# Kernel optimization log

Hardware: AMD Instinct MI355X
Metric: run time of the kernel (lower is better)

## Reference

```python
import jax, jax.numpy as jnp
import numpy as np

EPS = 1e-5

def _bn(x, g, b, m, v):
    # inference-mode batchnorm over channel axis 1
    s = (1, -1) + (1,) * (x.ndim - 2)
    return (x - m.reshape(s)) * (g.reshape(s) / jnp.sqrt(v.reshape(s) + EPS)) + b.reshape(s)

def _lrelu(x):
    return jnp.where(x >= 0, x, 0.2 * x)

def _graph_feature(x, k):
    # x: (B, C, N) -> (B, 2C, N, k): DGCNN cat([neighbor - center, center])
    xt = jnp.transpose(x, (0, 2, 1))                      # (B, N, C)
    sq = jnp.sum(xt * xt, axis=-1)                        # (B, N)
    neg_dist = 2.0 * jnp.einsum('bnc,bmc->bnm', xt, xt) - sq[:, :, None] - sq[:, None, :]
    idx = jax.lax.top_k(neg_dist, k)[1]                   # (B, N, k) nearest (incl. self)
    nb = jax.vmap(lambda f, i: f[i])(xt, idx)             # (B, N, k, C) neighbor gather
    ctr = jnp.broadcast_to(xt[:, :, None, :], nb.shape)
    feat = jnp.concatenate([nb - ctr, ctr], axis=-1)      # (B, N, k, 2C)
    return jnp.transpose(feat, (0, 3, 1, 2))

def _edge_conv(x, k, w, g, b, m, v):
    # 1x1 conv over edge features + BN + LeakyReLU(0.2) + max over k neighbors
    f = _graph_feature(x, k)
    h = jnp.einsum('oi,bink->bonk', w, f)
    return jnp.max(_lrelu(_bn(h, g, b, m, v)), axis=-1)   # (B, out, N)

def setup_inputs():
    key = jax.random.key(0)
    ks = jax.random.split(key, 40)
    rn = lambda i, s: jax.random.normal(ks[i], s, dtype=jnp.float32)
    ru = lambda i, s: jax.random.uniform(ks[i], s, dtype=jnp.float32)
    B, N, K = 8, 1024, 20
    inp = {'x': rn(0, (B, N, 3))}
    dims = [(64, 6), (64, 128), (128, 128), (256, 256)]
    for li, (o, ci) in enumerate(dims, 1):
        base = li * 5
        inp[f'c{li}w'] = rn(base, (o, ci)) * 0.2
        inp[f'c{li}g'] = ru(base + 1, (o,)) + 0.5
        inp[f'c{li}b'] = rn(base + 2, (o,)) * 0.1
        inp[f'c{li}m'] = rn(base + 3, (o,)) * 0.1
        inp[f'c{li}v'] = ru(base + 4, (o,)) + 0.5
    inp['f1w'] = rn(25, (128, 384)) * 0.05
    inp['f1b'] = rn(26, (128,)) * 0.1
    inp['n1g'] = ru(27, (128,)) + 0.5
    inp['n1b'] = rn(28, (128,)) * 0.1
    inp['n1m'] = rn(29, (128,)) * 0.1
    inp['n1v'] = ru(30, (128,)) + 0.5
    inp['f2w'] = rn(31, (16, 128)) * 0.1
    inp['f2b'] = rn(32, (16,)) * 0.1
    inp['n2g'] = ru(33, (16,)) + 0.5
    inp['n2b'] = rn(34, (16,)) * 0.1
    inp['n2m'] = rn(35, (16,)) * 0.1
    inp['n2v'] = ru(36, (16,)) + 0.5
    inp['f3w'] = rn(37, (1, 16)) * 0.2
    inp['f3b'] = rn(38, (1,)) * 0.1
    inp['k'] = K
    return inp

def reference(x, c1w, c1g, c1b, c1m, c1v, c2w, c2g, c2b, c2m, c2v,
              c3w, c3g, c3b, c3m, c3v, c4w, c4g, c4b, c4m, c4v,
              f1w, f1b, n1g, n1b, n1m, n1v, f2w, f2b, n2g, n2b, n2m, n2v,
              f3w, f3b, k):
    xt = jnp.transpose(x, (0, 2, 1))                       # (B, 3, N)
    h1 = _edge_conv(xt, k, c1w, c1g, c1b, c1m, c1v)        # (B, 64, N)
    h2 = _edge_conv(h1, k, c2w, c2g, c2b, c2m, c2v)        # (B, 64, N)
    h3 = _edge_conv(h2, k, c3w, c3g, c3b, c3m, c3v)        # (B, 128, N)
    h4 = _edge_conv(h3, k, c4w, c4g, c4b, c4m, c4v)        # (B, 256, N)
    p3 = jnp.max(h3, axis=-1)                              # global max pool over N
    p4 = jnp.max(h4, axis=-1)
    f = jnp.concatenate([p3, p4], axis=1)                  # (B, 384)
    f = jax.nn.relu(_bn(f @ f1w.T + f1b, n1g, n1b, n1m, n1v))
    f = jax.nn.relu(_bn(f @ f2w.T + f2b, n2g, n2b, n2m, n2v))
    return f @ f3w.T + f3b                                 # (B, 1)
```

## Files before the change

### kernel.cpp

```cpp
#include <hip/hip_runtime.h>
#include <math.h>

constexpr int B_ = 8;
constexpr int N_ = 1024;
constexpr int K_ = 20;
constexpr float EPS_ = 1e-5f;

typedef __attribute__((ext_vector_type(8))) short short8;
typedef __attribute__((ext_vector_type(4))) float f32x4;
typedef unsigned long long u64;

__device__ __forceinline__ void bf16split(float x, unsigned short& h, unsigned short& l) {
    unsigned u = __float_as_uint(x);
    unsigned rh = (u + 0x7FFFu + ((u >> 16) & 1u)) >> 16;
    h = (unsigned short)rh;
    float lof = x - __uint_as_float(rh << 16);
    unsigned ul = __float_as_uint(lof);
    l = (unsigned short)((ul + 0x7FFFu + ((ul >> 16) & 1u)) >> 16);
}

template <int CP>
__device__ __forceinline__ void distg_body(unsigned short* smem,
                                           const unsigned short* __restrict__ Hh,
                                           const unsigned short* __restrict__ Hl,
                                           const float* __restrict__ sq,
                                           float* __restrict__ dist, int bid) {
    constexpr int KC = CP / 32;
    constexpr int STR = 40;
    unsigned short* As = smem;
    unsigned short* Bs = smem + 2 * 128 * STR;
    int t = threadIdx.x;
    int bb = bid >> 6;
    int r0 = ((bid >> 3) & 7) * 128;
    int c0 = (bid & 7) * 128;
    size_t base = (size_t)bb * N_;
    int lane = t & 63, wave = t >> 6, quad = lane >> 4, nl = lane & 15;
    int wm = wave >> 1, wn = wave & 1;

    f32x4 acc[4][4];
#pragma unroll
    for (int mt = 0; mt < 4; ++mt)
#pragma unroll
        for (int nt = 0; nt < 4; ++nt) acc[mt][nt] = (f32x4){0.f, 0.f, 0.f, 0.f};

    for (int kc = 0; kc < KC; ++kc) {
        if (kc) __syncthreads();
#pragma unroll
        for (int i = 0; i < 2; ++i) {
            int cid = t + i * 256;
            int row = cid >> 2, j = cid & 3;
            size_t asrc = (base + r0 + row) * CP + kc * 32 + 8 * j;
            size_t bsrc = (base + c0 + row) * CP + kc * 32 + 8 * j;
            int dst = row * STR + 8 * j;
            *(short8*)&As[dst] = *(const short8*)&Hh[asrc];
            *(short8*)&As[128 * STR + dst] = *(const short8*)&Hl[asrc];
            *(short8*)&Bs[dst] = *(const short8*)&Hh[bsrc];
            *(short8*)&Bs[128 * STR + dst] = *(const short8*)&Hl[bsrc];
        }
        __syncthreads();
        short8 ah[4], al[4];
#pragma unroll
        for (int mt = 0; mt < 4; ++mt) {
            int off = (wm * 64 + mt * 16 + nl) * STR + quad * 8;
            ah[mt] = *(const short8*)&As[off];
            al[mt] = *(const short8*)&As[128 * STR + off];
        }
#pragma unroll
        for (int nt = 0; nt < 4; ++nt) {
            int off = (wn * 64 + nt * 16 + nl) * STR + quad * 8;
            short8 bh = *(const short8*)&Bs[off];
            short8 bl = *(const short8*)&Bs[128 * STR + off];
#pragma unroll
            for (int mt = 0; mt < 4; ++mt) {
                acc[mt][nt] = __builtin_amdgcn_mfma_f32_16x16x32_bf16(ah[mt], bh, acc[mt][nt], 0, 0, 0);
                acc[mt][nt] = __builtin_amdgcn_mfma_f32_16x16x32_bf16(ah[mt], bl, acc[mt][nt], 0, 0, 0);
                acc[mt][nt] = __builtin_amdgcn_mfma_f32_16x16x32_bf16(al[mt], bh, acc[mt][nt], 0, 0, 0);
            }
        }
    }
    float sqc[4];
#pragma unroll
    for (int nt = 0; nt < 4; ++nt) sqc[nt] = sq[base + c0 + wn * 64 + nt * 16 + nl];
    float* dbase = dist + (size_t)bb * N_ * N_;
#pragma unroll
    for (int mt = 0; mt < 4; ++mt) {
#pragma unroll
        for (int r = 0; r < 4; ++r) {
            int row = r0 + wm * 64 + mt * 16 + quad * 4 + r;
            float sqr = sq[base + row];
#pragma unroll
            for (int nt = 0; nt < 4; ++nt)
                dbase[(size_t)row * N_ + c0 + wn * 64 + nt * 16 + nl] =
                    2.f * acc[mt][nt][r] - sqr - sqc[nt];
        }
    }
}

template <int CP, int NOUT>
__device__ __forceinline__ void gemmyz_body(unsigned short* smem,
                                            const unsigned short* __restrict__ Hh,
                                            const unsigned short* __restrict__ Hl,
                                            const unsigned short* __restrict__ Wh,
                                            const unsigned short* __restrict__ Wl,
                                            const float* __restrict__ bias2,
                                            float* __restrict__ YZ, int yb) {
    constexpr int KC = CP / 32;
    constexpr int NTt = NOUT / 16;
    constexpr int STR = 40;
    unsigned short* As = smem;
    int t = threadIdx.x;
    int m0 = (yb & 63) * 128;
    int n0 = (yb >> 6) * 128;
    int lane = t & 63, wave = t >> 6, quad = lane >> 4, nl = lane & 15;
    int wm = wave >> 1, wn = wave & 1;

    f32x4 acc[4][4];
#pragma unroll
    for (int mt = 0; mt < 4; ++mt)
#pragma unroll
        for (int nt = 0; nt < 4; ++nt) acc[mt][nt] = (f32x4){0.f, 0.f, 0.f, 0.f};

    for (int kc = 0; kc < KC; ++kc) {
        if (kc) __syncthreads();
#pragma unroll
        for (int i = 0; i < 2; ++i) {
            int cid = t + i * 256;
            int row = cid >> 2, j = cid & 3;
            size_t src = ((size_t)(m0 + row)) * CP + kc * 32 + 8 * j;
            int dst = row * STR + 8 * j;
            *(short8*)&As[dst] = *(const short8*)&Hh[src];
            *(short8*)&As[128 * STR + dst] = *(const short8*)&Hl[src];
        }
        __syncthreads();
        short8 ah[4], al[4];
#pragma unroll
        for (int mt = 0; mt < 4; ++mt) {
            int off = (wm * 64 + mt * 16 + nl) * STR + quad * 8;
            ah[mt] = *(const short8*)&As[off];
            al[mt] = *(const short8*)&As[128 * STR + off];
        }
#pragma unroll
        for (int nt = 0; nt < 4; ++nt) {
            int ntg = (n0 >> 4) + wn * 4 + nt;
            size_t bpos = ((size_t)(kc * NTt + ntg) * 64 + lane) * 8;
            short8 bh = *(const short8*)&Wh[bpos];
            short8 bl = *(const short8*)&Wl[bpos];
#pragma unroll
            for (int mt = 0; mt < 4; ++mt) {
                acc[mt][nt] = __builtin_amdgcn_mfma_f32_16x16x32_bf16(ah[mt], bh, acc[mt][nt], 0, 0, 0);
                acc[mt][nt] = __builtin_amdgcn_mfma_f32_16x16x32_bf16(ah[mt], bl, acc[mt][nt], 0, 0, 0);
                acc[mt][nt] = __builtin_amdgcn_mfma_f32_16x16x32_bf16(al[mt], bh, acc[mt][nt], 0, 0, 0);
            }
        }
    }
#pragma unroll
    for (int nt = 0; nt < 4; ++nt) {
        int col = n0 + wn * 64 + nt * 16 + nl;
        float bv = bias2[col];
#pragma unroll
        for (int mt = 0; mt < 4; ++mt) {
#pragma unroll
            for (int r = 0; r < 4; ++r) {
                int row = m0 + wm * 64 + mt * 16 + quad * 4 + r;
                YZ[(size_t)row * NOUT + col] = acc[mt][nt][r] + bv;
            }
        }
    }
}

template <int CP, int NOUT>
__global__ __launch_bounds__(256) void distyz_kernel(const unsigned short* __restrict__ Hh,
                                                     const unsigned short* __restrict__ Hl,
                                                     const float* __restrict__ sq,
                                                     float* __restrict__ dist,
                                                     const unsigned short* __restrict__ Wh,
                                                     const unsigned short* __restrict__ Wl,
                                                     const float* __restrict__ bias2,
                                                     float* __restrict__ YZ) {
    __shared__ unsigned short smem[4 * 128 * 40];
    if (blockIdx.x < 512)
        distg_body<CP>(smem, Hh, Hl, sq, dist, blockIdx.x);
    else
        gemmyz_body<CP, NOUT>(smem, Hh, Hl, Wh, Wl, bias2, YZ, blockIdx.x - 512);
}

__global__ __launch_bounds__(256) void dist1y_kernel(const unsigned short* __restrict__ Hh,
                                                     const unsigned short* __restrict__ Hl,
                                                     const float* __restrict__ sq,
                                                     float* __restrict__ dist,
                                                     const float* __restrict__ x,
                                                     const float* __restrict__ wdT,
                                                     const float* __restrict__ wcdT,
                                                     const float* __restrict__ bias1,
                                                     float* __restrict__ YZ) {
    __shared__ unsigned short smem[4 * 128 * 40];
    if (blockIdx.x < 512) {
        distg_body<32>(smem, Hh, Hl, sq, dist, blockIdx.x);
    } else {
        int t = threadIdx.x;
        int p = (blockIdx.x - 512) * 4 + (t >> 6);
        int o = t & 63;
        float x0 = x[3 * p], x1 = x[3 * p + 1], x2 = x[3 * p + 2];
        float y = x0 * wdT[o] + x1 * wdT[64 + o] + x2 * wdT[128 + o];
        float z = bias1[o] + x0 * wcdT[o] + x1 * wcdT[64 + o] + x2 * wcdT[128 + o];
        YZ[(size_t)p * 128 + o] = y;
        YZ[(size_t)p * 128 + 64 + o] = z;
    }
}

__device__ __forceinline__ unsigned int fkey(float f) {
    unsigned int u = __float_as_uint(f);
    return (u & 0x80000000u) ? ~u : (u | 0x80000000u);
}

__device__ __forceinline__ u64 tree16(const u64* v) {
    u64 t0[8];
#pragma unroll
    for (int s = 0; s < 8; ++s) t0[s] = v[2 * s] > v[2 * s + 1] ? v[2 * s] : v[2 * s + 1];
#pragma unroll
    for (int s = 0; s < 4; ++s) t0[s] = t0[2 * s] > t0[2 * s + 1] ? t0[2 * s] : t0[2 * s + 1];
    t0[0] = t0[0] > t0[1] ? t0[0] : t0[1];
    t0[2] = t0[2] > t0[3] ? t0[2] : t0[3];
    return t0[0] > t0[2] ? t0[0] : t0[2];
}

__device__ __forceinline__ u64 wave_sort_desc(u64 v, int lane) {
#pragma unroll
    for (int k2 = 2; k2 <= 64; k2 <<= 1) {
#pragma unroll
        for (int j = k2 >> 1; j > 0; j >>= 1) {
            u64 o = __shfl_xor(v, j);
            bool desc = ((lane & k2) == 0);
            bool lower = ((lane & j) == 0);
            u64 mx = v > o ? v : o;
            u64 mn = v > o ? o : v;
            v = (desc == lower) ? mx : mn;
        }
    }
    return v;
}

__device__ __forceinline__ void sel_row(const float* __restrict__ d, int* nidxrow,
                                        u64* candbuf, int lane) {
    int c0 = lane * 16;
    u64 kk[16];
#pragma unroll
    for (int i = 0; i < 4; ++i) {
        float4 a = *(const float4*)&d[c0 + 4 * i];
        float av[4] = {a.x, a.y, a.z, a.w};
#pragma unroll
        for (int e = 0; e < 4; ++e) {
            int c = c0 + 4 * i + e;
            kk[4 * i + e] = ((u64)fkey(av[e]) << 32) | (unsigned int)(~c);
        }
    }
    u64 lm = tree16(kk);
    u64 lms = wave_sort_desc(lm, lane);
    u64 tau = __shfl(lms, 19);

    int cnt = 0;
#pragma unroll
    for (int i = 0; i < 16; ++i) cnt += (kk[i] >= tau) ? 1 : 0;
    int incl = cnt;
#pragma unroll
    for (int dd = 1; dd < 64; dd <<= 1) {
        int n = __shfl_up(incl, dd);
        if (lane >= dd) incl += n;
    }
    int excl = incl - cnt;
    int Ctot = __shfl(incl, 63);

    if (Ctot <= 64) {
        candbuf[lane] = 0ull;
        __builtin_amdgcn_wave_barrier();
        int pos = excl;
#pragma unroll
        for (int i = 0; i < 16; ++i) {
            if (kk[i] >= tau) { candbuf[pos] = kk[i]; ++pos; }
        }
        __builtin_amdgcn_wave_barrier();
        u64 c = candbuf[lane];
        c = wave_sort_desc(c, lane);
        if (lane < K_) nidxrow[lane] = (int)(~(unsigned int)c);
    } else {
        for (int it = 0; it < K_; ++it) {
            u64 m = tree16(kk);
#pragma unroll
            for (int off = 32; off; off >>= 1) {
                u64 o = __shfl_xor(m, off);
                m = o > m ? o : m;
            }
            if (lane == 0) nidxrow[it] = (int)(~(unsigned int)m);
#pragma unroll
            for (int j = 0; j < 16; ++j) kk[j] = (kk[j] == m) ? 0ull : kk[j];
        }
    }
}

template <int COUT, bool WRITE_H, bool WRITE_NEXT>
__global__ __launch_bounds__(256) void selgmx_kernel(const float* __restrict__ dist,
                                                     const float* __restrict__ YZ,
                                                     unsigned short* __restrict__ Hh,
                                                     unsigned short* __restrict__ Hl,
                                                     float* __restrict__ sq,
                                                     float* __restrict__ h) {
    constexpr int NOUT = 2 * COUT;
    constexpr int PPG = 256 / COUT;
    __shared__ int nidx[PPG][K_];
    __shared__ u64 cand[PPG][64];
    __shared__ float part[4];
    int t = threadIdx.x, wave = t >> 6, lane = t & 63;
    int p0 = blockIdx.x * PPG;

    if (wave < PPG)
        sel_row(dist + (size_t)(p0 + wave) * N_, nidx[wave], cand[wave], lane);
    __syncthreads();

    int pg = t / COUT, o = t % COUT, p = p0 + pg;
    size_t ybase = (size_t)(p >> 10) << 10;
    float m = -INFINITY;
#pragma unroll
    for (int k = 0; k < K_; ++k)
        m = fmaxf(m, YZ[(ybase + nidx[pg][k]) * NOUT + o]);
    float val = m + YZ[(size_t)p * NOUT + COUT + o];
    val = (val >= 0.f) ? val : 0.2f * val;
    if constexpr (WRITE_H) h[(size_t)p * COUT + o] = val;
    if constexpr (WRITE_NEXT) {
        unsigned short hi, lo;
        bf16split(val, hi, lo);
        Hh[(size_t)p * COUT + o] = hi;
        Hl[(size_t)p * COUT + o] = lo;
        float s = val * val;
#pragma unroll
        for (int d = 32; d; d >>= 1) s += __shfl_xor(s, d);
        if (lane == 0) part[wave] = s;
        __syncthreads();
        if (t < PPG) {
            constexpr int WPP = COUT / 64;
            float tot = 0.f;
#pragma unroll
            for (int w2 = 0; w2 < WPP; ++w2) tot += part[t * WPP + w2];
            sq[p0 + t] = tot;
        }
    }
}

__device__ __forceinline__ void prep_mfma2_elem(int e, int CIN, int COUT_,
                                                const float* w, const float* g,
                                                const float* bb, const float* m,
                                                const float* v,
                                                unsigned short* Wh, unsigned short* Wl,
                                                float* bias2) {
    int NOUT = 2 * COUT_;
    int NT = NOUT / 16;
    int n = e % NOUT, k = e / NOUT;
    int o = (n < COUT_) ? n : n - COUT_;
    float a = g[o] / sqrtf(v[o] + EPS_);
    float wv = (n < COUT_) ? a * w[o * 2 * CIN + k]
                           : a * (w[o * 2 * CIN + CIN + k] - w[o * 2 * CIN + k]);
    unsigned short hs, ls;
    bf16split(wv, hs, ls);
    int kc = k >> 5, ko = k & 31, quad = ko >> 3, j = ko & 7;
    int nt = n >> 4, nl = n & 15;
    size_t pos = ((size_t)(kc * NT + nt) * 64 + quad * 16 + nl) * 8 + j;
    Wh[pos] = hs;
    Wl[pos] = ls;
    if (k == 0) bias2[n] = (n < COUT_) ? 0.f : (bb[o] - m[o] * a);
}

__global__ __launch_bounds__(256) void setup_kernel(
    const float* __restrict__ x, unsigned short* __restrict__ Hh,
    unsigned short* __restrict__ Hl, float* __restrict__ sq,
    const float* __restrict__ w1, const float* __restrict__ g1, const float* __restrict__ bb1,
    const float* __restrict__ m1, const float* __restrict__ v1,
    const float* __restrict__ w2, const float* __restrict__ g2, const float* __restrict__ bb2,
    const float* __restrict__ m2, const float* __restrict__ v2,
    const float* __restrict__ w3, const float* __restrict__ g3, const float* __restrict__ bb3,
    const float* __restrict__ m3, const float* __restrict__ v3,
    const float* __restrict__ w4, const float* __restrict__ g4, const float* __restrict__ bb4,
    const float* __restrict__ m4, const float* __restrict__ v4,
    float* __restrict__ wd, float* __restrict__ wcd, float* __restrict__ bias1,
    unsigned short* __restrict__ Wh2, unsigned short* __restrict__ Wl2, float* __restrict__ b22,
    unsigned short* __restrict__ Wh3, unsigned short* __restrict__ Wl3, float* __restrict__ b23,
    unsigned short* __restrict__ Wh4, unsigned short* __restrict__ Wl4, float* __restrict__ b24) {
    int t = threadIdx.x;
    if (blockIdx.x < 32) {
        int p = blockIdx.x * 256 + t;
        const float* r = x + (size_t)p * 3;
        unsigned short hb[32], lb[32];
        float s = 0.f;
#pragma unroll
        for (int c = 0; c < 3; ++c) {
            float v = r[c];
            s += v * v;
            bf16split(v, hb[c], lb[c]);
        }
#pragma unroll
        for (int c = 3; c < 32; ++c) { hb[c] = 0; lb[c] = 0; }
        sq[p] = s;
#pragma unroll
        for (int i = 0; i < 4; ++i) {
            *(short8*)&Hh[(size_t)p * 32 + 8 * i] = *(const short8*)&hb[8 * i];
            *(short8*)&Hl[(size_t)p * 32 + 8 * i] = *(const short8*)&lb[8 * i];
        }
        return;
    }
    int e = (blockIdx.x - 32) * 256 + t;
    if (e < 192) {
        int o = e % 64, i = e / 64;
        float a = g1[o] / sqrtf(v1[o] + EPS_);
        float wdv = w1[o * 6 + i];
        wd[e] = a * wdv;
        wcd[e] = a * (w1[o * 6 + 3 + i] - wdv);
        if (i == 0) bias1[o] = bb1[o] - m1[o] * a;
    } else if (e < 192 + 8192) {
        prep_mfma2_elem(e - 192, 64, 64, w2, g2, bb2, m2, v2, Wh2, Wl2, b22);
    } else if (e < 192 + 8192 + 16384) {
        prep_mfma2_elem(e - 8384, 64, 128, w3, g3, bb3, m3, v3, Wh3, Wl3, b23);
    } else if (e < 192 + 8192 + 16384 + 65536) {
        prep_mfma2_elem(e - 24768, 128, 256, w4, g4, bb4, m4, v4, Wh4, Wl4, b24);
    }
}

__global__ __launch_bounds__(256) void pool1_all(const float* __restrict__ h3,
                                                 const float* __restrict__ h4,
                                                 float* __restrict__ p128,
                                                 float* __restrict__ p256) {
    __shared__ float red[4][64];
    int bid = blockIdx.x;
    const float* h;
    float* part;
    int C, bb, cb, z;
    if (bid < 256) {
        z = bid & 15; cb = (bid >> 4) & 1; bb = bid >> 5;
        C = 128; h = h3; part = p128;
    } else {
        int e = bid - 256;
        z = e & 15; cb = (e >> 4) & 3; bb = e >> 6;
        C = 256; h = h4; part = p256;
    }
    int lane = threadIdx.x & 63, sl = threadIdx.x >> 6;
    int c = cb * 64 + lane;
    const float* hb = h + (size_t)bb * N_ * C;
    int n0 = z * 64 + sl * 16;
    float mx = -INFINITY;
#pragma unroll
    for (int i = 0; i < 16; ++i) mx = fmaxf(mx, hb[(size_t)(n0 + i) * C + c]);
    red[sl][lane] = mx;
    __syncthreads();
    if (sl == 0) {
        mx = fmaxf(fmaxf(red[0][lane], red[1][lane]), fmaxf(red[2][lane], red[3][lane]));
        part[((size_t)bb * 16 + z) * C + c] = mx;
    }
}

__global__ __launch_bounds__(64) void pool2_all(const float* __restrict__ p128,
                                                const float* __restrict__ p256,
                                                float* __restrict__ f) {
    int bid = blockIdx.x;
    const float* part;
    int C, bb, cb, off;
    if (bid < 16) { cb = bid & 1; bb = bid >> 1; C = 128; part = p128; off = 0; }
    else { int e = bid - 16; cb = e & 3; bb = e >> 2; C = 256; part = p256; off = 128; }
    int c = cb * 64 + threadIdx.x;
    float mx = -INFINITY;
#pragma unroll
    for (int z = 0; z < 16; ++z)
        mx = fmaxf(mx, part[((size_t)bb * 16 + z) * C + c]);
    f[bb * 384 + off + c] = mx;
}

__global__ __launch_bounds__(128) void fc_tail(
    const float* __restrict__ f, const float* __restrict__ f1w,
    const float* __restrict__ f1b, const float* __restrict__ n1g,
    const float* __restrict__ n1b, const float* __restrict__ n1m,
    const float* __restrict__ n1v, const float* __restrict__ f2w,
    const float* __restrict__ f2b, const float* __restrict__ n2g,
    const float* __restrict__ n2b, const float* __restrict__ n2m,
    const float* __restrict__ n2v, const float* __restrict__ f3w,
    const float* __restrict__ f3b, float* __restrict__ out) {
    __shared__ float fb[384];
    __shared__ float s1[128];
    __shared__ float s2[16];
    int bb = blockIdx.x, t = threadIdx.x;
    for (int j = t; j < 384; j += 128) fb[j] = f[bb * 384 + j];
    __syncthreads();
    float a = f1b[t];
    for (int j = 0; j < 384; ++j) a += f1w[t * 384 + j] * fb[j];
    a = (a - n1m[t]) * (n1g[t] / sqrtf(n1v[t] + EPS_)) + n1b[t];
    s1[t] = fmaxf(a, 0.f);
    __syncthreads();
    if (t < 16) {
        float a2 = f2b[t];
        for (int j = 0; j < 128; ++j) a2 += f2w[t * 128 + j] * s1[j];
        a2 = (a2 - n2m[t]) * (n2g[t] / sqrtf(n2v[t] + EPS_)) + n2b[t];
        s2[t] = fmaxf(a2, 0.f);
    }
    __syncthreads();
    if (t == 0) {
        float a3 = f3b[0];
        for (int j = 0; j < 16; ++j) a3 += f3w[j] * s2[j];
        out[bb] = a3;
    }
}

extern "C" void kernel_launch(void* const* d_in, const int* in_sizes, int n_in,
                              void* d_out, int out_size, void* d_ws, size_t ws_size,
                              hipStream_t stream) {
    const float* x = (const float*)d_in[0];
    const float* cw[4] = {(const float*)d_in[1], (const float*)d_in[6],
                          (const float*)d_in[11], (const float*)d_in[16]};
    const float* cg[4] = {(const float*)d_in[2], (const float*)d_in[7],
                          (const float*)d_in[12], (const float*)d_in[17]};
    const float* cb[4] = {(const float*)d_in[3], (const float*)d_in[8],
                          (const float*)d_in[13], (const float*)d_in[18]};
    const float* cm[4] = {(const float*)d_in[4], (const float*)d_in[9],
                          (const float*)d_in[14], (const float*)d_in[19]};
    const float* cv[4] = {(const float*)d_in[5], (const float*)d_in[10],
                          (const float*)d_in[15], (const float*)d_in[20]};
    const float* f1w = (const float*)d_in[21];
    const float* f1b = (const float*)d_in[22];
    const float* n1g = (const float*)d_in[23];
    const float* n1b = (const float*)d_in[24];
    const float* n1m = (const float*)d_in[25];
    const float* n1v = (const float*)d_in[26];
    const float* f2w = (const float*)d_in[27];
    const float* f2b = (const float*)d_in[28];
    const float* n2g = (const float*)d_in[29];
    const float* n2b = (const float*)d_in[30];
    const float* n2m = (const float*)d_in[31];
    const float* n2v = (const float*)d_in[32];
    const float* f3w = (const float*)d_in[33];
    const float* f3b = (const float*)d_in[34];
    float* out = (float*)d_out;

    char* ws = (char*)d_ws;
    size_t off = 0;
    auto alloc = [&](size_t bytes) {
        void* p = ws + off;
        off += (bytes + 255) & ~(size_t)255;
        return p;
    };
    float* sq = (float*)alloc(B_ * N_ * 4);
    float* h3 = (float*)alloc((size_t)B_ * N_ * 128 * 4);
    float* h4 = (float*)alloc((size_t)B_ * N_ * 256 * 4);
    float* wd = (float*)alloc(3 * 64 * 4);
    float* wcd = (float*)alloc(3 * 64 * 4);
    float* bias1 = (float*)alloc(64 * 4);
    float* b22 = (float*)alloc(128 * 4);
    float* b23 = (float*)alloc(256 * 4);
    float* b24 = (float*)alloc(512 * 4);
    float* f = (float*)alloc(B_ * 384 * 4);
    float* p128 = (float*)alloc((size_t)B_ * 16 * 128 * 4);
    float* p256 = (float*)alloc((size_t)B_ * 16 * 256 * 4);
    unsigned short* Wh2 = (unsigned short*)alloc(64 * 128 * 2);
    unsigned short* Wl2 = (unsigned short*)alloc(64 * 128 * 2);
    unsigned short* Wh3 = (unsigned short*)alloc(64 * 256 * 2);
    unsigned short* Wl3 = (unsigned short*)alloc(64 * 256 * 2);
    unsigned short* Wh4 = (unsigned short*)alloc(128 * 512 * 2);
    unsigned short* Wl4 = (unsigned short*)alloc(128 * 512 * 2);
    unsigned short* Hh = (unsigned short*)alloc((size_t)B_ * N_ * 128 * 2);
    unsigned short* Hl = (unsigned short*)alloc((size_t)B_ * N_ * 128 * 2);
    float* dist = (float*)alloc((size_t)B_ * N_ * N_ * 4);
    float* YZ = (float*)alloc((size_t)B_ * N_ * 512 * 4);
    (void)ws_size; (void)in_sizes; (void)n_in; (void)out_size;

    setup_kernel<<<32 + (192 + 8192 + 16384 + 65536 + 255) / 256, 256, 0, stream>>>(
        x, Hh, Hl, sq,
        cw[0], cg[0], cb[0], cm[0], cv[0], cw[1], cg[1], cb[1], cm[1], cv[1],
        cw[2], cg[2], cb[2], cm[2], cv[2], cw[3], cg[3], cb[3], cm[3], cv[3],
        wd, wcd, bias1, Wh2, Wl2, b22, Wh3, Wl3, b23, Wh4, Wl4, b24);

    dist1y_kernel<<<512 + 2048, 256, 0, stream>>>(Hh, Hl, sq, dist, x, wd, wcd, bias1, YZ);
    selgmx_kernel<64, false, true><<<B_ * N_ / 4, 256, 0, stream>>>(dist, YZ, Hh, Hl, sq, nullptr);

    distyz_kernel<64, 128><<<512 + 64, 256, 0, stream>>>(Hh, Hl, sq, dist, Wh2, Wl2, b22, YZ);
    selgmx_kernel<64, false, true><<<B_ * N_ / 4, 256, 0, stream>>>(dist, YZ, Hh, Hl, sq, nullptr);

    distyz_kernel<64, 256><<<512 + 128, 256, 0, stream>>>(Hh, Hl, sq, dist, Wh3, Wl3, b23, YZ);
    selgmx_kernel<128, true, true><<<B_ * N_ / 2, 256, 0, stream>>>(dist, YZ, Hh, Hl, sq, h3);

    distyz_kernel<128, 512><<<512 + 256, 256, 0, stream>>>(Hh, Hl, sq, dist, Wh4, Wl4, b24, YZ);
    selgmx_kernel<256, true, false><<<B_ * N_, 256, 0, stream>>>(dist, YZ, nullptr, nullptr, nullptr, h4);

    pool1_all<<<256 + 512, 256, 0, stream>>>(h3, h4, p128, p256);
    pool2_all<<<16 + 32, 64, 0, stream>>>(p128, p256, f);
    fc_tail<<<B_, 128, 0, stream>>>(f, f1w, f1b, n1g, n1b, n1m, n1v, f2w, f2b, n2g, n2b,
                                    n2m, n2v, f3w, f3b, out);
}
```

Before: 284.8 us.

## Interleave batches across block IDs and fold final pooling into fc tail

Reorders the block-to-work mapping in the distance, GEMM, first-layer and selection kernels so consecutive block IDs cycle through the 8 batches. Adjacent blocks then touch different batches' data, which may spread traffic across memory channels and XCD L2 caches on MI355X (round-robin dispatch). The second pooling kernel is removed and its max-reduction moved into the fc tail, dropping one launch and an intermediate buffer. Locality of neighbouring blocks sharing rows changes, which could hurt cache reuse.

After: 272.9 us (median of 2 runs). 4.2% less time.

```diff
diff --git a/kernel.cpp b/kernel.cpp
--- a/kernel.cpp
+++ b/kernel.cpp
@@ -30,9 +30,9 @@
     unsigned short* As = smem;
     unsigned short* Bs = smem + 2 * 128 * STR;
     int t = threadIdx.x;
-    int bb = bid >> 6;
-    int r0 = ((bid >> 3) & 7) * 128;
-    int c0 = (bid & 7) * 128;
+    int bb = bid & 7;
+    int r0 = ((bid >> 6) & 7) * 128;
+    int c0 = ((bid >> 3) & 7) * 128;
     size_t base = (size_t)bb * N_;
     int lane = t & 63, wave = t >> 6, quad = lane >> 4, nl = lane & 15;
     int wm = wave >> 1, wn = wave & 1;
@@ -109,8 +109,9 @@
     constexpr int STR = 40;
     unsigned short* As = smem;
     int t = threadIdx.x;
-    int m0 = (yb & 63) * 128;
-    int n0 = (yb >> 6) * 128;
+    int q = yb & 7, mband = (yb >> 3) & 7, ntile = yb >> 6;
+    int m0 = (q * 8 + mband) * 128;
+    int n0 = ntile * 128;
     int lane = t & 63, wave = t >> 6, quad = lane >> 4, nl = lane & 15;
     int wm = wave >> 1, wn = wave & 1;
 
@@ -197,8 +198,9 @@
     if (blockIdx.x < 512) {
         distg_body<32>(smem, Hh, Hl, sq, dist, blockIdx.x);
     } else {
+        int bid2 = blockIdx.x - 512;
         int t = threadIdx.x;
-        int p = (blockIdx.x - 512) * 4 + (t >> 6);
+        int p = ((bid2 & 7) << 10) + ((bid2 >> 3) * 4) + (t >> 6);
         int o = t & 63;
         float x0 = x[3 * p], x1 = x[3 * p + 1], x2 = x[3 * p + 2];
         float y = x0 * wdT[o] + x1 * wdT[64 + o] + x2 * wdT[128 + o];
@@ -310,7 +312,7 @@
     __shared__ u64 cand[PPG][64];
     __shared__ float part[4];
     int t = threadIdx.x, wave = t >> 6, lane = t & 63;
-    int p0 = blockIdx.x * PPG;
+    int p0 = ((blockIdx.x & 7) << 10) + (blockIdx.x >> 3) * PPG;
 
     if (wave < PPG)
         sel_row(dist + (size_t)(p0 + wave) * N_, nidx[wave], cand[wave], lane);
@@ -454,24 +456,9 @@
     }
 }
 
-__global__ __launch_bounds__(64) void pool2_all(const float* __restrict__ p128,
-                                                const float* __restrict__ p256,
-                                                float* __restrict__ f) {
-    int bid = blockIdx.x;
-    const float* part;
-    int C, bb, cb, off;
-    if (bid < 16) { cb = bid & 1; bb = bid >> 1; C = 128; part = p128; off = 0; }
-    else { int e = bid - 16; cb = e & 3; bb = e >> 2; C = 256; part = p256; off = 128; }
-    int c = cb * 64 + threadIdx.x;
-    float mx = -INFINITY;
-#pragma unroll
-    for (int z = 0; z < 16; ++z)
-        mx = fmaxf(mx, part[((size_t)bb * 16 + z) * C + c]);
-    f[bb * 384 + off + c] = mx;
-}
-
 __global__ __launch_bounds__(128) void fc_tail(
-    const float* __restrict__ f, const float* __restrict__ f1w,
+    const float* __restrict__ p128, const float* __restrict__ p256,
+    const float* __restrict__ f1w,
     const float* __restrict__ f1b, const float* __restrict__ n1g,
     const float* __restrict__ n1b, const float* __restrict__ n1m,
     const float* __restrict__ n1v, const float* __restrict__ f2w,
@@ -483,7 +470,20 @@
     __shared__ float s1[128];
     __shared__ float s2[16];
     int bb = blockIdx.x, t = threadIdx.x;
-    for (int j = t; j < 384; j += 128) fb[j] = f[bb * 384 + j];
+    for (int j = t; j < 384; j += 128) {
+        float mx = -INFINITY;
+        if (j < 128) {
+#pragma unroll
+            for (int z = 0; z < 16; ++z)
+                mx = fmaxf(mx, p128[((size_t)bb * 16 + z) * 128 + j]);
+        } else {
+            int c = j - 128;
+#pragma unroll
+            for (int z = 0; z < 16; ++z)
+                mx = fmaxf(mx, p256[((size_t)bb * 16 + z) * 256 + c]);
+        }
+        fb[j] = mx;
+    }
     __syncthreads();
     float a = f1b[t];
     for (int j = 0; j < 384; ++j) a += f1w[t * 384 + j] * fb[j];
@@ -550,7 +550,6 @@
     float* b22 = (float*)alloc(128 * 4);
     float* b23 = (float*)alloc(256 * 4);
     float* b24 = (float*)alloc(512 * 4);
-    float* f = (float*)alloc(B_ * 384 * 4);
     float* p128 = (float*)alloc((size_t)B_ * 16 * 128 * 4);
     float* p256 = (float*)alloc((size_t)B_ * 16 * 256 * 4);
     unsigned short* Wh2 = (unsigned short*)alloc(64 * 128 * 2);
@@ -584,7 +583,6 @@
     selgmx_kernel<256, true, false><<<B_ * N_, 256, 0, stream>>>(dist, YZ, nullptr, nullptr, nullptr, h4);
 
     pool1_all<<<256 + 512, 256, 0, stream>>>(h3, h4, p128, p256);
-    pool2_all<<<16 + 32, 64, 0, stream>>>(p128, p256, f);
-    fc_tail<<<B_, 128, 0, stream>>>(f, f1w, f1b, n1g, n1b, n1m, n1v, f2w, f2b, n2g, n2b,
-                                    n2m, n2v, f3w, f3b, out);
-}
+    fc_tail<<<B_, 128, 0, stream>>>(p128, p256, f1w, f1b, n1g, n1b, n1m, n1v, f2w, f2b,
+                                    n2g, n2b, n2m, n2v, f3w, f3b, out);
+}
```
